# Kernel optimization log

Measured on AMD Instinct MI355X. Metric: run time of the kernel, lower is better.

## Reference

```python
import jax, jax.numpy as jnp
import numpy as np
from jax import lax

B, C, D, H, W = 4, 384, 16, 16, 16
DSTATE, DCONV, EXPAND = 16, 4, 2
DIN = C * EXPAND            # 768
DTRANK = (C + 15) // 16     # 24
EPS = 1e-5


def setup_inputs() -> dict:
    ks = jax.random.split(jax.random.key(0), 12)
    g = lambda k, shape, s=0.02: jax.random.normal(k, shape, jnp.float32) * s
    return {
        "x": jax.random.normal(ks[0], (B, C, D, H, W), jnp.float32),
        "gsc_w1": g(ks[1], (C, C, 3, 3, 3)), "gsc_b1": jnp.zeros((C,), jnp.float32),
        "gsc_w2": g(ks[2], (C, C, 3, 3, 3)), "gsc_b2": jnp.zeros((C,), jnp.float32),
        "gsc_w3": g(ks[3], (C, C, 1, 1, 1)), "gsc_b3": jnp.zeros((C,), jnp.float32),
        "gsc_w4": g(ks[4], (C, C, 1, 1, 1)), "gsc_b4": jnp.zeros((C,), jnp.float32),
        "ln_g": jnp.ones((C,), jnp.float32), "ln_b": jnp.zeros((C,), jnp.float32),
        "in_proj_w": g(ks[5], (2 * DIN, C)),
        "conv1d_w": g(ks[6], (DIN, 1, DCONV), 0.1), "conv1d_b": jnp.zeros((DIN,), jnp.float32),
        "x_proj_w": g(ks[7], (DTRANK + 2 * DSTATE, DIN)),
        "dt_proj_w": g(ks[8], (DIN, DTRANK), 0.1), "dt_proj_b": jnp.full((DIN,), -4.0, jnp.float32),
        "A_log": jnp.log(jnp.tile(jnp.arange(1, DSTATE + 1, dtype=jnp.float32), (DIN, 1))),
        "D_skip": jnp.ones((DIN,), jnp.float32),
        "out_proj_w": g(ks[9], (C, DIN)),
    }


def _conv3d(x, w, b, pad):
    y = lax.conv_general_dilated(x, w, (1, 1, 1), [(pad, pad)] * 3,
                                 dimension_numbers=("NCDHW", "OIDHW", "NCDHW"))
    return y + b[None, :, None, None, None]


def _inorm(x):  # InstanceNorm3d, affine=False, biased variance
    m = x.mean((2, 3, 4), keepdims=True)
    v = x.var((2, 3, 4), keepdims=True)
    return (x - m) * lax.rsqrt(v + EPS)


def _forward(x, gsc_w1, gsc_b1, gsc_w2, gsc_b2, gsc_w3, gsc_b3, gsc_w4, gsc_b4,
             ln_g, ln_b, in_proj_w, conv1d_w, conv1d_b, x_proj_w,
             dt_proj_w, dt_proj_b, A_log, D_skip, out_proj_w):
    relu = jax.nn.relu
    # ---- GSC block (residual gated spatial conv) ----
    x1 = relu(_inorm(_conv3d(x, gsc_w1, gsc_b1, 1)))
    x1 = relu(_inorm(_conv3d(x1, gsc_w2, gsc_b2, 1)))
    x2 = relu(_inorm(_conv3d(x, gsc_w3, gsc_b3, 0)))
    xg = relu(_inorm(_conv3d(x1 + x2, gsc_w4, gsc_b4, 0))) + x
    # ---- MambaLayer: flatten voxels to tokens ----
    Bn = xg.shape[0]
    L = D * H * W
    t = xg.reshape(Bn, C, L).swapaxes(1, 2)                     # [B, L, C]
    mu = t.mean(-1, keepdims=True)
    var = t.var(-1, keepdims=True)
    tn = (t - mu) * lax.rsqrt(var + EPS) * ln_g + ln_b          # LayerNorm
    # ---- Mamba block ----
    xz = tn @ in_proj_w.T                                       # [B, L, 2*DIN]
    xin, z = jnp.split(xz, 2, axis=-1)
    xc = xin.swapaxes(1, 2)                                     # [B, DIN, L]
    xc = lax.conv_general_dilated(xc, conv1d_w, (1,), [(DCONV - 1, 0)],
                                  dimension_numbers=("NCH", "OIH", "NCH"),
                                  feature_group_count=DIN)      # causal depthwise conv
    u = jax.nn.silu(xc + conv1d_b[None, :, None]).swapaxes(1, 2)  # [B, L, DIN]
    dbl = u @ x_proj_w.T                                        # [B, L, DTRANK+2N]
    dt, Bm, Cm = jnp.split(dbl, [DTRANK, DTRANK + DSTATE], axis=-1)
    dt = jax.nn.softplus(dt @ dt_proj_w.T + dt_proj_b)          # [B, L, DIN]
    A = -jnp.exp(A_log)                                         # [DIN, N]

    def step(h, inp):  # h: [B, DIN, N]
        dt_t, B_t, C_t, u_t = inp
        dA = jnp.exp(dt_t[:, :, None] * A)
        h = dA * h + (dt_t * u_t)[:, :, None] * B_t[:, None, :]
        return h, jnp.einsum("bdn,bn->bd", h, C_t)

    h0 = jnp.zeros((Bn, DIN, DSTATE), x.dtype)
    _, ys = lax.scan(step, h0, (dt.swapaxes(0, 1), Bm.swapaxes(0, 1),
                                Cm.swapaxes(0, 1), u.swapaxes(0, 1)))
    y = ys.swapaxes(0, 1) + u * D_skip                          # [B, L, DIN]
    y = y * jax.nn.silu(z)
    out = y @ out_proj_w.T                                      # [B, L, C]
    return out.swapaxes(1, 2).reshape(Bn, C, D, H, W)


def reference(x, gsc_w1, gsc_b1, gsc_w2, gsc_b2, gsc_w3, gsc_b3, gsc_w4, gsc_b4,
              ln_g, ln_b, in_proj_w, conv1d_w, conv1d_b, x_proj_w,
              dt_proj_w, dt_proj_b, A_log, D_skip, out_proj_w):
    return _forward(x, gsc_w1, gsc_b1, gsc_w2, gsc_b2, gsc_w3, gsc_b3, gsc_w4, gsc_b4,
                    ln_g, ln_b, in_proj_w, conv1d_w, conv1d_b, x_proj_w,
                    dt_proj_w, dt_proj_b, A_log, D_skip, out_proj_w)
```

## Files before the change

### kernel.cpp

```cpp
#include <hip/hip_runtime.h>
#include <math.h>

#define CDIM 384
#define SDIM 4096
#define BDIM 4
#define DINC 768
#define NST  16
#define NCHUNK 64
#define LCHUNK 64
#define PSTRIDE 6291456

typedef unsigned short ushort_t;
typedef unsigned int uint_t;
typedef __attribute__((ext_vector_type(4))) float f32x4;
typedef __attribute__((ext_vector_type(8))) short bf16x8;

__device__ __forceinline__ ushort_t f2bf(float f) {
    union { float f; uint_t u; } v; v.f = f;
    uint_t r = v.u + 0x7FFFu + ((v.u >> 16) & 1u);
    return (ushort_t)(r >> 16);
}
__device__ __forceinline__ float bf2f(ushort_t u) {
    union { uint_t i; float f; } v; v.i = ((uint_t)u) << 16; return v.f;
}
__device__ __forceinline__ uint_t pk2(float a, float b) {
    return (uint_t)f2bf(a) | ((uint_t)f2bf(b) << 16);
}

__device__ __forceinline__ void wconv_body(const float* __restrict__ W,
                                           ushort_t* __restrict__ Wb, int idx) {
    const float* wp = W + (size_t)idx * 27;
#pragma unroll
    for (int tap = 0; tap < 27; ++tap)
        Wb[(size_t)tap * (CDIM * CDIM) + idx] = f2bf(wp[tap]);
}
__device__ __forceinline__ void cvt_body(const float* __restrict__ src,
                                         ushort_t* __restrict__ dst, int i) {
    float4 v = ((const float4*)src)[i];
    uint2 o; o.x = pk2(v.x, v.y); o.y = pk2(v.z, v.w);
    ((uint2*)dst)[i] = o;
}
__global__ __launch_bounds__(256)
void prep_weights_kernel(const float* w1, const float* w2, const float* w3,
                         const float* w4, const float* ipw, const float* opw,
                         const float* xpw,
                         ushort_t* Wb1, ushort_t* Wb2, ushort_t* w3b, ushort_t* w4b,
                         ushort_t* ipwb, ushort_t* opwb, ushort_t* xpwb) {
    const int bid = blockIdx.x, t = threadIdx.x;
    if      (bid < 576)  wconv_body(w1, Wb1, bid * 256 + t);
    else if (bid < 1152) wconv_body(w2, Wb2, (bid - 576) * 256 + t);
    else if (bid < 1296) cvt_body(w3, w3b, (bid - 1152) * 256 + t);
    else if (bid < 1440) cvt_body(w4, w4b, (bid - 1296) * 256 + t);
    else if (bid < 2016) cvt_body(ipw, ipwb, (bid - 1440) * 256 + t);
    else if (bid < 2304) cvt_body(opw, opwb, (bid - 2016) * 256 + t);
    else                 cvt_body(xpw, xpwb, (bid - 2304) * 256 + t);
}

__global__ __launch_bounds__(384)
void pad_kernel(const float* __restrict__ src, ushort_t* __restrict__ Xp) {
    const int blk = blockIdx.x;
    const int b = blk >> 8, d = (blk >> 4) & 15, h = blk & 15;
    const int ci = threadIdx.x;
    const float* sp = src + (size_t)(b * CDIM + ci) * SDIM + d * 256 + h * 16;
    ushort_t* dp = Xp + ((((size_t)(b * 18 + d + 1) * 18) + (h + 1)) * 18 + 1) * CDIM + ci;
#pragma unroll
    for (int w = 0; w < 16; ++w)
        dp[(size_t)w * CDIM] = f2bf(sp[w]);
}

__global__ __launch_bounds__(384)
void pad_fuse2_kernel(const float* __restrict__ P0, const float* __restrict__ P1,
                      const float* __restrict__ stats, ushort_t* __restrict__ Xp) {
    const int blk = blockIdx.x;
    const int b = blk >> 8, d = (blk >> 4) & 15, h = blk & 15;
    const int ci = threadIdx.x;
    const size_t o = (size_t)(b * CDIM + ci) * SDIM + d * 256 + h * 16;
    const float m = stats[(b * CDIM + ci) * 2], r = stats[(b * CDIM + ci) * 2 + 1];
    ushort_t* dp = Xp + ((((size_t)(b * 18 + d + 1) * 18) + (h + 1)) * 18 + 1) * CDIM + ci;
#pragma unroll
    for (int w = 0; w < 16; ++w) {
        const float v = P0[o + w] + P1[o + w];
        dp[(size_t)w * CDIM] = f2bf(fmaxf((v - m) * r, 0.f));
    }
}

__global__ __launch_bounds__(384)
void pad_fuse3_kernel(const float* __restrict__ P0, const float* __restrict__ P1,
                      const float* __restrict__ st2, const float* __restrict__ C3,
                      const float* __restrict__ st3, ushort_t* __restrict__ Xp) {
    const int blk = blockIdx.x;
    const int b = blk >> 8, d = (blk >> 4) & 15, h = blk & 15;
    const int ci = threadIdx.x;
    const size_t o = (size_t)(b * CDIM + ci) * SDIM + d * 256 + h * 16;
    const float m2 = st2[(b * CDIM + ci) * 2], r2 = st2[(b * CDIM + ci) * 2 + 1];
    const float m3 = st3[(b * CDIM + ci) * 2], r3 = st3[(b * CDIM + ci) * 2 + 1];
    ushort_t* dp = Xp + ((((size_t)(b * 18 + d + 1) * 18) + (h + 1)) * 18 + 1) * CDIM + ci;
#pragma unroll
    for (int w = 0; w < 16; ++w) {
        const float x1 = fmaxf((P0[o + w] + P1[o + w] - m2) * r2, 0.f);
        const float x2 = fmaxf((C3[o + w] - m3) * r3, 0.f);
        dp[(size_t)w * CDIM] = f2bf(x1 + x2);
    }
}

template<int MODE>
__global__ __launch_bounds__(256)
void conv_kernel(const ushort_t* __restrict__ Xp, const ushort_t* __restrict__ Wb,
                 const ushort_t* __restrict__ W3, float* __restrict__ Y01,
                 float* __restrict__ Y2) {
    constexpr int NZ = (MODE == 0) ? 2 : (MODE == 1 ? 3 : 1);
    const int cpx = gridDim.x >> 3;
    const int lin = blockIdx.x;
    const int wid = (lin & 7) * cpx + (lin >> 3);
    const int co0 = (wid % 3) * 128;
    const int zz  = (wid / 3) % NZ;
    const int ntid = wid / (3 * NZ);
    const int b  = ntid >> 5;
    const int d  = (ntid >> 1) & 15;
    const int h0 = (ntid & 1) * 8;
    const int t = threadIdx.x;
    const int lane = t & 63;
    const int wy = (t >> 6) >> 1, wx = (t >> 6) & 1;

    const bool is1x1 = (MODE == 2) || (MODE == 1 && zz == 2);
    const ushort_t* Wsrc; int tap0, iters, kd0, kh0, kw0; float* Y;
    if (is1x1) {
        Wsrc = W3; tap0 = 0; iters = 12; kd0 = 1; kh0 = 1; kw0 = 1; Y = Y2;
    } else {
        Wsrc = Wb; tap0 = zz ? 14 : 0; iters = (zz ? 13 : 14) * 12;
        kd0 = zz ? 1 : 0; kh0 = zz ? 1 : 0; kw0 = zz ? 2 : 0;
        Y = Y01 + (size_t)zz * PSTRIDE;
    }

    __shared__ ushort_t As[2][128 * 40];
    __shared__ ushort_t Bs[2][128 * 40];

    f32x4 acc[4][4];
#pragma unroll
    for (int i = 0; i < 4; ++i)
#pragma unroll
        for (int j = 0; j < 4; ++j) acc[i][j] = (f32x4){0.f, 0.f, 0.f, 0.f};

    const int arow = t >> 1, half = t & 1;
    const int hl = arow >> 4, w = arow & 15;
    const int wA = arow * 40 + half * 16;

    const int lm = lane & 15, lk = (lane >> 4) * 8;
    const int rA0 = (wy * 64 + lm) * 40 + lk;
    const int rB0 = (wx * 64 + lm) * 40 + lk;

    const ushort_t* ap = Wsrc + (size_t)tap0 * (CDIM * CDIM)
                       + (size_t)(co0 + arow) * CDIM + half * 16;
    const ushort_t* bp = Xp + ((((size_t)(b * 18 + d + kd0) * 18) + (h0 + hl + kh0)) * 18
                               + (w + kw0)) * CDIM + half * 16;
    int c12 = 0, ckw = kw0, ckh = kh0;

    uint4 ra0, ra1, rb0, rb1;

    auto loadg = [&]() {
        const uint4* pa = reinterpret_cast<const uint4*>(ap);
        ra0 = pa[0]; ra1 = pa[1];
        const uint4* pb = reinterpret_cast<const uint4*>(bp);
        rb0 = pb[0]; rb1 = pb[1];
        ap += 32; bp += 32;
        if (++c12 == 12) {
            c12 = 0;
            ap += CDIM * CDIM - 384;
            if (++ckw == 3) {
                ckw = 0;
                if (++ckh == 3) { ckh = 0; bp += 109440; }
                else bp += 5760;
            }
        }
    };
    auto lwrite = [&](int buf) {
        *reinterpret_cast<uint4*>(&As[buf][wA])     = ra0;
        *reinterpret_cast<uint4*>(&As[buf][wA + 8]) = ra1;
        *reinterpret_cast<uint4*>(&Bs[buf][wA])     = rb0;
        *reinterpret_cast<uint4*>(&Bs[buf][wA + 8]) = rb1;
    };

    loadg();
    lwrite(0);
    __syncthreads();

    int buf = 0;
    for (int idx = 0; idx < iters; ++idx) {
        const bool more = (idx + 1) < iters;
        if (more) loadg();
        bf16x8 af[4], bfr[4];
#pragma unroll
        for (int mi = 0; mi < 4; ++mi)
            af[mi] = *reinterpret_cast<const bf16x8*>(&As[buf][rA0 + mi * 640]);
#pragma unroll
        for (int ni = 0; ni < 4; ++ni)
            bfr[ni] = *reinterpret_cast<const bf16x8*>(&Bs[buf][rB0 + ni * 640]);
#pragma unroll
        for (int mi = 0; mi < 4; ++mi)
#pragma unroll
            for (int ni = 0; ni < 4; ++ni)
                acc[mi][ni] = __builtin_amdgcn_mfma_f32_16x16x32_bf16(
                    af[mi], bfr[ni], acc[mi][ni], 0, 0, 0);
        if (more) lwrite(buf ^ 1);
        __syncthreads();
        buf ^= 1;
    }

    const int coB = co0 + wy * 64 + (lane >> 4) * 4;
    const int nB  = wx * 64 + lm;
#pragma unroll
    for (int mi = 0; mi < 4; ++mi) {
#pragma unroll
        for (int ni = 0; ni < 4; ++ni) {
            const int nl = nB + ni * 16;
            const int s = d * 256 + (h0 + (nl >> 4)) * 16 + (nl & 15);
            float* yp = Y + ((size_t)b * CDIM + (coB + mi * 16)) * SDIM + s;
#pragma unroll
            for (int j = 0; j < 4; ++j)
                yp[(size_t)j * SDIM] = acc[mi][ni][j];
        }
    }
}

template<int EPI>
__global__ __launch_bounds__(256)
void gemm_mfma_kernel(const ushort_t* __restrict__ A, const ushort_t* __restrict__ Bw,
                      void* __restrict__ Cv, void* __restrict__ C2v,
                      int M, int N, int K, int ldc, int nx) {
    const int cpx = gridDim.x >> 3;
    const int lin = blockIdx.x;
    const int wid = (lin & 7) * cpx + (lin >> 3);
    const int n0 = (wid % nx) * 128;
    const int m0 = (wid / nx) * 128;
    const int t = threadIdx.x;
    const int lane = t & 63;
    const int wy = (t >> 6) >> 1, wx = (t >> 6) & 1;

    __shared__ ushort_t As[2][128 * 40];
    __shared__ ushort_t Bs[2][128 * 40];

    f32x4 acc[4][4];
#pragma unroll
    for (int i = 0; i < 4; ++i)
#pragma unroll
        for (int j = 0; j < 4; ++j) acc[i][j] = (f32x4){0.f, 0.f, 0.f, 0.f};

    const int arow = t >> 1, half = t & 1;
    const int wA = arow * 40 + half * 16;
    const int lm = lane & 15, lk = (lane >> 4) * 8;
    const int rA0 = (wy * 64 + lm) * 40 + lk;
    const int rB0 = (wx * 64 + lm) * 40 + lk;

    uint4 ra0, ra1, rb0, rb1;

    auto loadg = [&](int kk) {
        const int kb = kk * 32 + half * 16;
        const uint4* pa = reinterpret_cast<const uint4*>(
            A + (size_t)(m0 + arow) * K + kb);
        ra0 = pa[0]; ra1 = pa[1];
        if (n0 + arow < N) {
            const uint4* pb = reinterpret_cast<const uint4*>(
                Bw + (size_t)(n0 + arow) * K + kb);
            rb0 = pb[0]; rb1 = pb[1];
        } else {
            rb0 = make_uint4(0, 0, 0, 0); rb1 = rb0;
        }
    };
    auto lwrite = [&](int buf) {
        *reinterpret_cast<uint4*>(&As[buf][wA])     = ra0;
        *reinterpret_cast<uint4*>(&As[buf][wA + 8]) = ra1;
        *reinterpret_cast<uint4*>(&Bs[buf][wA])     = rb0;
        *reinterpret_cast<uint4*>(&Bs[buf][wA + 8]) = rb1;
    };

    const int KI = K >> 5;
    loadg(0);
    lwrite(0);
    __syncthreads();

    int buf = 0;
    for (int kk = 0; kk < KI; ++kk) {
        const bool more = (kk + 1) < KI;
        if (more) loadg(kk + 1);
        bf16x8 af[4], bfr[4];
#pragma unroll
        for (int mi = 0; mi < 4; ++mi)
            af[mi] = *reinterpret_cast<const bf16x8*>(&As[buf][rA0 + mi * 640]);
#pragma unroll
        for (int ni = 0; ni < 4; ++ni)
            bfr[ni] = *reinterpret_cast<const bf16x8*>(&Bs[buf][rB0 + ni * 640]);
#pragma unroll
        for (int mi = 0; mi < 4; ++mi)
#pragma unroll
            for (int ni = 0; ni < 4; ++ni)
                acc[mi][ni] = __builtin_amdgcn_mfma_f32_16x16x32_bf16(
                    af[mi], bfr[ni], acc[mi][ni], 0, 0, 0);
        if (more) lwrite(buf ^ 1);
        __syncthreads();
        buf ^= 1;
    }

    const int mB = m0 + wy * 64 + (lane >> 4) * 4;
    const int nB = n0 + wx * 64 + lm;
#pragma unroll
    for (int mi = 0; mi < 4; ++mi) {
#pragma unroll
        for (int ni = 0; ni < 4; ++ni) {
            const int n = nB + ni * 16;
            if (EPI == 2) {
                const int mrow = mB + mi * 16;
                const int bb = mrow >> 12, l = mrow & 4095;
                float4 st = {acc[mi][ni][0], acc[mi][ni][1],
                             acc[mi][ni][2], acc[mi][ni][3]};
                *reinterpret_cast<float4*>(
                    (float*)Cv + ((size_t)(bb * CDIM + n)) * SDIM + l) = st;
            } else {
#pragma unroll
                for (int j = 0; j < 4; ++j) {
                    const int m = mB + mi * 16 + j;
                    const float v = acc[mi][ni][j];
                    if (EPI == 0) {
                        if (n < N) ((float*)Cv)[(size_t)m * ldc + n] = v;
                    } else {
                        if (n < DINC) ((ushort_t*)Cv)[(size_t)m * DINC + n] = f2bf(v);
                        else ((ushort_t*)C2v)[(size_t)m * DINC + (n - DINC)] = f2bf(v);
                    }
                }
            }
        }
    }
}

__device__ __forceinline__ void stats_reduce(float s, float ss, float* out) {
#pragma unroll
    for (int off = 32; off > 0; off >>= 1) {
        s += __shfl_down(s, off);
        ss += __shfl_down(ss, off);
    }
    __shared__ float rs[4], rss[4];
    const int wid = threadIdx.x >> 6;
    if ((threadIdx.x & 63) == 0) { rs[wid] = s; rss[wid] = ss; }
    __syncthreads();
    if (threadIdx.x == 0) {
        float S = rs[0] + rs[1] + rs[2] + rs[3];
        float SS = rss[0] + rss[1] + rss[2] + rss[3];
        float m = S * (1.f / SDIM);
        float var = SS * (1.f / SDIM) - m * m;
        out[0] = m;
        out[1] = rsqrtf(var + 1e-5f);
    }
}

__global__ __launch_bounds__(256)
void inorm_stats_combo_kernel(const float* __restrict__ P0, const float* __restrict__ P1,
                              float* __restrict__ SA, const float* __restrict__ X3,
                              float* __restrict__ SB) {
    const int bid = blockIdx.x;
    float s = 0.f, ss = 0.f;
    if (bid < 1536) {
        const float* p0 = P0 + (size_t)bid * SDIM;
        const float* p1 = P1 + (size_t)bid * SDIM;
        for (int i = threadIdx.x * 4; i < SDIM; i += 1024) {
            float4 a = *(const float4*)(p0 + i);
            float4 c = *(const float4*)(p1 + i);
            const float vx = a.x + c.x, vy = a.y + c.y, vz = a.z + c.z, vw = a.w + c.w;
            s += vx + vy + vz + vw;
            ss += vx * vx + vy * vy + vz * vz + vw * vw;
        }
        stats_reduce(s, ss, SA + bid * 2);
    } else {
        const int bc = bid - 1536;
        const float* xp = X3 + (size_t)bc * SDIM;
        for (int i = threadIdx.x * 4; i < SDIM; i += 1024) {
            float4 v = *(const float4*)(xp + i);
            s += v.x + v.y + v.z + v.w;
            ss += v.x * v.x + v.y * v.y + v.z * v.z + v.w * v.w;
        }
        stats_reduce(s, ss, SB + bc * 2);
    }
}

__global__ __launch_bounds__(256)
void inorm_stats_kernel(const float* __restrict__ X, float* __restrict__ stats) {
    const int bc = blockIdx.x;
    const float* xp = X + (size_t)bc * SDIM;
    float s = 0.f, ss = 0.f;
    for (int i = threadIdx.x * 4; i < SDIM; i += 1024) {
        float4 v = *(const float4*)(xp + i);
        s += v.x + v.y + v.z + v.w;
        ss += v.x * v.x + v.y * v.y + v.z * v.z + v.w * v.w;
    }
    stats_reduce(s, ss, stats + bc * 2);
}

__global__ __launch_bounds__(256)
void layernorm_kernel(const float* __restrict__ C4, const float* __restrict__ stats,
                      const float* __restrict__ X, const float* __restrict__ gam,
                      const float* __restrict__ bet, ushort_t* __restrict__ Tn) {
    const int token = blockIdx.x * 4 + (threadIdx.x >> 6);
    const int lane = threadIdx.x & 63;
    const int b = token >> 12, l = token & 4095;
    const size_t base = (size_t)b * CDIM * SDIM + l;
    float v[6];
    float s = 0.f, ss = 0.f;
#pragma unroll
    for (int i = 0; i < 6; ++i) {
        const int c = lane + i * 64;
        const size_t o = base + (size_t)c * SDIM;
        const float m = stats[(b * CDIM + c) * 2], r = stats[(b * CDIM + c) * 2 + 1];
        v[i] = fmaxf((C4[o] - m) * r, 0.f) + X[o];
        s += v[i]; ss += v[i] * v[i];
    }
#pragma unroll
    for (int off = 32; off > 0; off >>= 1) {
        s += __shfl_down(s, off);
        ss += __shfl_down(ss, off);
    }
    s = __shfl(s, 0); ss = __shfl(ss, 0);
    const float m = s * (1.f / CDIM);
    const float r = rsqrtf(ss * (1.f / CDIM) - m * m + 1e-5f);
    ushort_t* tp = Tn + (size_t)token * CDIM;
#pragma unroll
    for (int i = 0; i < 6; ++i) {
        const int c = lane + i * 64;
        tp[c] = f2bf((v[i] - m) * r * gam[c] + bet[c]);
    }
}

__global__ __launch_bounds__(256)
void gemm_dtproj_kernel(const float* __restrict__ A, const float* __restrict__ B,
                        ushort_t* __restrict__ C, const float* __restrict__ bias,
                        int M, int N, int K, int lda, int ldb, int ldc) {
    __shared__ __align__(16) float As[16][132];
    __shared__ __align__(16) float Bs[16][68];
    const int t = threadIdx.x;
    const int m0 = blockIdx.y * 128;
    const int n0 = blockIdx.x * 64;

    float acc[8][4];
#pragma unroll
    for (int i = 0; i < 8; ++i)
#pragma unroll
        for (int j = 0; j < 4; ++j) acc[i][j] = 0.f;

    const int mr = (t & 15) * 8;
    const int nr = (t >> 4) * 4;

    for (int k0 = 0; k0 < K; k0 += 16) {
#pragma unroll
        for (int idx = 0; idx < 8; ++idx) {
            const int e = idx * 256 + t;
            const int k = e & 15, m = e >> 4;
            float v = 0.f;
            if (k0 + k < K) v = A[(size_t)(m0 + m) * lda + (k0 + k)];
            As[k][m] = v;
        }
#pragma unroll
        for (int idx = 0; idx < 4; ++idx) {
            const int e = idx * 256 + t;
            const int k = e & 15, n = e >> 4;
            float v = 0.f;
            if ((n0 + n) < N && (k0 + k) < K) v = B[(size_t)(n0 + n) * ldb + (k0 + k)];
            Bs[k][n] = v;
        }
        __syncthreads();
#pragma unroll
        for (int k = 0; k < 16; ++k) {
            float4 a0 = *(const float4*)&As[k][mr];
            float4 a1 = *(const float4*)&As[k][mr + 4];
            float4 b0 = *(const float4*)&Bs[k][nr];
            const float av[8] = {a0.x, a0.y, a0.z, a0.w, a1.x, a1.y, a1.z, a1.w};
            const float bv[4] = {b0.x, b0.y, b0.z, b0.w};
#pragma unroll
            for (int i = 0; i < 8; ++i)
#pragma unroll
                for (int j = 0; j < 4; ++j)
                    acc[i][j] = fmaf(av[i], bv[j], acc[i][j]);
        }
        __syncthreads();
    }

#pragma unroll
    for (int i = 0; i < 8; ++i) {
        const int m = m0 + mr + i;
#pragma unroll
        for (int j = 0; j < 4; ++j) {
            const int n = n0 + nr + j;
            if (n >= N) continue;
            float v = acc[i][j] + bias[n];
            v = (v > 20.f) ? v : log1pf(__expf(v));
            C[(size_t)m * ldc + n] = f2bf(v);
        }
    }
}

__global__ __launch_bounds__(256)
void dwconv_silu_kernel(const ushort_t* __restrict__ Xin, const float* __restrict__ W,
                        const float* __restrict__ bias, ushort_t* __restrict__ U) {
    const int dch = blockIdx.x * 256 + threadIdx.x;
    const int l0 = blockIdx.y * 4, b = blockIdx.z;
    const float4 w4 = ((const float4*)W)[dch];
    const float wk[4] = {w4.x, w4.y, w4.z, w4.w};
    const float bs = bias[dch];
    const size_t base = ((size_t)b * 4096 + l0) * DINC + dch;
    float r[7];
#pragma unroll
    for (int k = 0; k < 7; ++k) {
        const int ll = l0 - 3 + k;
        r[k] = (ll >= 0) ? bf2f(Xin[base + (size_t)(k - 3) * DINC]) : 0.f;
    }
#pragma unroll
    for (int j = 0; j < 4; ++j) {
        float acc = bs;
#pragma unroll
        for (int k = 0; k < 4; ++k) acc = fmaf(r[j + k], wk[k], acc);
        U[base + (size_t)j * DINC] = f2bf(acc / (1.f + __expf(-acc)));
    }
}

__global__ __launch_bounds__(256)
void scan_phase1_kernel(const ushort_t* __restrict__ DT, const ushort_t* __restrict__ U,
                        const float* __restrict__ DBL, const float* __restrict__ A_log,
                        float* __restrict__ HOUT, float* __restrict__ SDT) {
    const int b = blockIdx.z, chunk = blockIdx.y;
    const int dch = blockIdx.x * 256 + threadIdx.x;
    float Arow[16];
#pragma unroll
    for (int n = 0; n < NST; ++n) Arow[n] = -__expf(A_log[dch * NST + n]);

    __shared__ float bcs[LCHUNK][16];
    const size_t tokbase = (size_t)b * 4096 + chunk * LCHUNK;
#pragma unroll
    for (int idx = 0; idx < 4; ++idx) {
        const int e = idx * 256 + threadIdx.x;
        bcs[e >> 4][e & 15] = DBL[(tokbase + (e >> 4)) * 56 + 24 + (e & 15)];
    }
    __syncthreads();

    size_t off = tokbase * DINC + dch;
    float h[16];
#pragma unroll
    for (int n = 0; n < NST; ++n) h[n] = 0.f;
    float sdt = 0.f;
    float cdt = bf2f(DT[off]), cu = bf2f(U[off]);
    for (int t = 0; t < LCHUNK; ++t) {
        float ndt = 0.f, nu = 0.f;
        if (t < LCHUNK - 1) { ndt = bf2f(DT[off + DINC]); nu = bf2f(U[off + DINC]); }
        sdt += cdt;
        const float du = cdt * cu;
#pragma unroll
        for (int n = 0; n < NST; ++n)
            h[n] = __expf(cdt * Arow[n]) * h[n] + du * bcs[t][n];
        off += DINC;
        cdt = ndt; cu = nu;
    }
    float* hp = HOUT + (((size_t)(b * DINC + dch) * NCHUNK + chunk) << 4);
#pragma unroll
    for (int n = 0; n < NST; ++n) hp[n] = h[n];
    SDT[(size_t)(b * DINC + dch) * NCHUNK + chunk] = sdt;
}

__global__ __launch_bounds__(256)
void scan_phase2_kernel(float* __restrict__ HOUT, const float* __restrict__ SDT,
                        const float* __restrict__ A_log) {
    const int t = blockIdx.x * 256 + threadIdx.x;
    const int b = t / (DINC * NST);
    const int rem = t - b * (DINC * NST);
    const int d = rem >> 4, n = rem & 15;
    const float An = -__expf(A_log[d * NST + n]);
    float* hp = HOUT + (((size_t)(b * DINC + d) * NCHUNK) << 4) + n;
    const float* sp = SDT + (size_t)(b * DINC + d) * NCHUNK;
    float H = 0.f;
    for (int c = 0; c < NCHUNK; ++c) {
        const float tmp = hp[c * 16];
        const float dA = __expf(An * sp[c]);
        hp[c * 16] = H;
        H = dA * H + tmp;
    }
}

__global__ __launch_bounds__(256)
void scan_phase3_kernel(ushort_t* __restrict__ DT, const ushort_t* __restrict__ U,
                        const float* __restrict__ DBL, const ushort_t* __restrict__ Z,
                        const float* __restrict__ A_log, const float* __restrict__ D_skip,
                        const float* __restrict__ HOUT) {
    const int b = blockIdx.z, chunk = blockIdx.y;
    const int dch = blockIdx.x * 256 + threadIdx.x;
    float Arow[16];
#pragma unroll
    for (int n = 0; n < NST; ++n) Arow[n] = -__expf(A_log[dch * NST + n]);
    const float Dsk = D_skip[dch];

    __shared__ float bcs[LCHUNK][32];
    const size_t tokbase = (size_t)b * 4096 + chunk * LCHUNK;
#pragma unroll
    for (int idx = 0; idx < 8; ++idx) {
        const int e = idx * 256 + threadIdx.x;
        bcs[e >> 5][e & 31] = DBL[(tokbase + (e >> 5)) * 56 + 24 + (e & 31)];
    }
    __syncthreads();

    float h[16];
    const float* hp = HOUT + (((size_t)(b * DINC + dch) * NCHUNK + chunk) << 4);
#pragma unroll
    for (int n = 0; n < NST; ++n) h[n] = hp[n];

    size_t off = tokbase * DINC + dch;
    float cdt = bf2f(DT[off]), cu = bf2f(U[off]), cz = bf2f(Z[off]);
    for (int t = 0; t < LCHUNK; ++t) {
        float ndt = 0.f, nu = 0.f, nz = 0.f;
        if (t < LCHUNK - 1) {
            ndt = bf2f(DT[off + DINC]); nu = bf2f(U[off + DINC]); nz = bf2f(Z[off + DINC]);
        }
        const float du = cdt * cu;
        float y = 0.f;
#pragma unroll
        for (int n = 0; n < NST; ++n) {
            h[n] = __expf(cdt * Arow[n]) * h[n] + du * bcs[t][n];
            y = fmaf(h[n], bcs[t][16 + n], y);
        }
        y += cu * Dsk;
        const float sz = cz / (1.f + __expf(-cz));
        DT[off] = f2bf(y * sz);
        off += DINC;
        cdt = ndt; cu = nu; cz = nz;
    }
}

extern "C" void kernel_launch(void* const* d_in, const int* in_sizes, int n_in,
                              void* d_out, int out_size, void* d_ws, size_t ws_size,
                              hipStream_t stream) {
    (void)in_sizes; (void)n_in; (void)out_size; (void)ws_size;
    const float* x         = (const float*)d_in[0];
    const float* w1        = (const float*)d_in[1];
    const float* w2        = (const float*)d_in[3];
    const float* w3        = (const float*)d_in[5];
    const float* w4        = (const float*)d_in[7];
    const float* ln_g      = (const float*)d_in[9];
    const float* ln_b      = (const float*)d_in[10];
    const float* in_proj_w = (const float*)d_in[11];
    const float* conv1d_w  = (const float*)d_in[12];
    const float* conv1d_b  = (const float*)d_in[13];
    const float* x_proj_w  = (const float*)d_in[14];
    const float* dt_proj_w = (const float*)d_in[15];
    const float* dt_proj_b = (const float*)d_in[16];
    const float* A_log     = (const float*)d_in[17];
    const float* D_skip    = (const float*)d_in[18];
    const float* out_proj_w= (const float*)d_in[19];
    float* out = (float*)d_out;

    float* ws = (float*)d_ws;
    float* R0 = ws;
    float* R1 = ws + 6291456;
    float* R2 = ws + 12582912;
    float* R3 = ws + 25165824;
    float* R4 = ws + 37748736;

    float*    P0    = R0;
    float*    P1    = R1;
    ushort_t* Wb1   = (ushort_t*)R2;
    ushort_t* Xp    = (ushort_t*)(R2 + 2097152);
    ushort_t* w3b   = (ushort_t*)(R2 + 6576128);
    ushort_t* w4b   = (ushort_t*)(R2 + 6649856);
    ushort_t* Wb2   = (ushort_t*)(R2 + 6723584);
    float*    SA    = R4;
    float*    SB    = R4 + 4096;
    ushort_t* ipwb  = (ushort_t*)(R4 + 6291456);
    ushort_t* opwb  = (ushort_t*)(R4 + 6586368);
    ushort_t* xpwb  = (ushort_t*)(R4 + 6733824);
    ushort_t* tnb   = (ushort_t*)R0;
    float*    DBL   = R0 + 3145728;
    float*    HOUT  = R1;
    float*    SDT   = R1 + 3145728;
    ushort_t* XIN   = (ushort_t*)R2;
    ushort_t* Zb    = (ushort_t*)R3;
    ushort_t* Ub    = (ushort_t*)R4;
    ushort_t* DTb   = (ushort_t*)R2;

    const size_t XP_BYTES = (size_t)4 * 18 * 18 * 18 * CDIM * 2;

    hipMemsetAsync(Xp, 0, XP_BYTES, stream);
    prep_weights_kernel<<<2346, 256, 0, stream>>>(
        w1, w2, w3, w4, in_proj_w, out_proj_w, x_proj_w,
        Wb1, Wb2, w3b, w4b, ipwb, opwb, xpwb);
    pad_kernel<<<1024, 384, 0, stream>>>(x, Xp);
    conv_kernel<1><<<1152, 256, 0, stream>>>(Xp, Wb1, w3b, P0, R3);
    inorm_stats_combo_kernel<<<3072, 256, 0, stream>>>(P0, P1, SA, R3, SB);
    pad_fuse2_kernel<<<1024, 384, 0, stream>>>(P0, P1, SA, Xp);
    conv_kernel<0><<<768, 256, 0, stream>>>(Xp, Wb2, nullptr, P0, nullptr);
    inorm_stats_combo_kernel<<<1536, 256, 0, stream>>>(P0, P1, SA, nullptr, nullptr);
    pad_fuse3_kernel<<<1024, 384, 0, stream>>>(P0, P1, SA, R3, SB, Xp);
    conv_kernel<2><<<384, 256, 0, stream>>>(Xp, nullptr, w4b, nullptr, R3);
    inorm_stats_kernel<<<1536, 256, 0, stream>>>(R3, SA);
    layernorm_kernel<<<4096, 256, 0, stream>>>(R3, SA, x, ln_g, ln_b, tnb);
    gemm_mfma_kernel<1><<<1536, 256, 0, stream>>>(
        tnb, ipwb, XIN, Zb, 16384, 1536, CDIM, 0, 12);
    dwconv_silu_kernel<<<dim3(3, 1024, 4), 256, 0, stream>>>(XIN, conv1d_w, conv1d_b, Ub);
    gemm_mfma_kernel<0><<<128, 256, 0, stream>>>(
        Ub, xpwb, DBL, nullptr, 16384, 56, DINC, 56, 1);
    gemm_dtproj_kernel<<<dim3(12, 128), 256, 0, stream>>>(
        DBL, dt_proj_w, DTb, dt_proj_b, 16384, DINC, 24, 56, 24, DINC);
    scan_phase1_kernel<<<dim3(3, NCHUNK, 4), 256, 0, stream>>>(
        DTb, Ub, DBL, A_log, HOUT, SDT);
    scan_phase2_kernel<<<192, 256, 0, stream>>>(HOUT, SDT, A_log);
    scan_phase3_kernel<<<dim3(3, NCHUNK, 4), 256, 0, stream>>>(
        DTb, Ub, DBL, Zb, A_log, D_skip, HOUT);
    gemm_mfma_kernel<2><<<384, 256, 0, stream>>>(
        DTb, opwb, out, nullptr, 16384, CDIM, DINC, 0, 3);
}
```

Baseline: 892.1 us.

## Load conv tiles directly into LDS with swizzle, drop XCD block remap

The implicit-GEMM conv kernel now uses global_load_lds to copy A and B tiles straight into a single-buffered, XOR-swizzled LDS tile with no padding, replacing register-staged double buffering. Blocks are reordered so spatial tiles vary fastest, and the XCD-aware block remapping is removed from both the conv and GEMM kernels. This cuts VGPR pressure and LDS footprint, which may raise occupancy. It also gives up the overlap of global loads with MFMA work inside a block and adds a second barrier per iteration.

Result: faster. 810.2 us (-9.2%).

```diff
diff --git a/kernel.cpp b/kernel.cpp
--- a/kernel.cpp
+++ b/kernel.cpp
@@ -25,6 +25,11 @@
 }
 __device__ __forceinline__ uint_t pk2(float a, float b) {
     return (uint_t)f2bf(a) | ((uint_t)f2bf(b) << 16);
+}
+__device__ __forceinline__ void gl16(const ushort_t* g, ushort_t* l) {
+    __builtin_amdgcn_global_load_lds(
+        (const __attribute__((address_space(1))) void*)(g),
+        (__attribute__((address_space(3))) void*)(l), 16, 0, 0);
 }
 
 __device__ __forceinline__ void wconv_body(const float* __restrict__ W,
@@ -108,19 +113,18 @@
 void conv_kernel(const ushort_t* __restrict__ Xp, const ushort_t* __restrict__ Wb,
                  const ushort_t* __restrict__ W3, float* __restrict__ Y01,
                  float* __restrict__ Y2) {
-    constexpr int NZ = (MODE == 0) ? 2 : (MODE == 1 ? 3 : 1);
-    const int cpx = gridDim.x >> 3;
-    const int lin = blockIdx.x;
-    const int wid = (lin & 7) * cpx + (lin >> 3);
-    const int co0 = (wid % 3) * 128;
-    const int zz  = (wid / 3) % NZ;
-    const int ntid = wid / (3 * NZ);
+    const int wid = blockIdx.x;
+    const int ntid = wid & 127;
+    const int rest = wid >> 7;
+    const int co0 = (rest % 3) * 128;
+    const int zz  = rest / 3;
     const int b  = ntid >> 5;
     const int d  = (ntid >> 1) & 15;
     const int h0 = (ntid & 1) * 8;
     const int t = threadIdx.x;
     const int lane = t & 63;
-    const int wy = (t >> 6) >> 1, wx = (t >> 6) & 1;
+    const int wv = t >> 6;
+    const int wy = wv >> 1, wx = wv & 1;
 
     const bool is1x1 = (MODE == 2) || (MODE == 1 && zz == 2);
     const ushort_t* Wsrc; int tap0, iters, kd0, kh0, kw0; float* Y;
@@ -132,8 +136,8 @@
         Y = Y01 + (size_t)zz * PSTRIDE;
     }
 
-    __shared__ ushort_t As[2][128 * 40];
-    __shared__ ushort_t Bs[2][128 * 40];
+    __shared__ __align__(16) ushort_t As[4096];
+    __shared__ __align__(16) ushort_t Bs[4096];
 
     f32x4 acc[4][4];
 #pragma unroll
@@ -141,69 +145,58 @@
 #pragma unroll
         for (int j = 0; j < 4; ++j) acc[i][j] = (f32x4){0.f, 0.f, 0.f, 0.f};
 
-    const int arow = t >> 1, half = t & 1;
-    const int hl = arow >> 4, w = arow & 15;
-    const int wA = arow * 40 + half * 16;
-
-    const int lm = lane & 15, lk = (lane >> 4) * 8;
-    const int rA0 = (wy * 64 + lm) * 40 + lk;
-    const int rB0 = (wx * 64 + lm) * 40 + lk;
-
-    const ushort_t* ap = Wsrc + (size_t)tap0 * (CDIM * CDIM)
-                       + (size_t)(co0 + arow) * CDIM + half * 16;
-    const ushort_t* bp = Xp + ((((size_t)(b * 18 + d + kd0) * 18) + (h0 + hl + kh0)) * 18
-                               + (w + kw0)) * CDIM + half * 16;
+    const int l4 = lane >> 2;
+    const int cg = (((lane & 3) ^ ((lane >> 3) & 3)) << 3);
+    int aTC[2], bTC[2];
+#pragma unroll
+    for (int i = 0; i < 2; ++i) {
+        const int r = wv * 32 + i * 16 + l4;
+        aTC[i] = (co0 + r) * CDIM + cg;
+        bTC[i] = ((r >> 4) * 18 + (r & 15)) * CDIM + cg;
+    }
+    ushort_t* lA[2] = { &As[wv * 1024], &As[wv * 1024 + 512] };
+    ushort_t* lB[2] = { &Bs[wv * 1024], &Bs[wv * 1024 + 512] };
+
+    int aoff = tap0 * (CDIM * CDIM);
+    int goff = (((b * 18 + d + kd0) * 18 + (h0 + kh0)) * 18 + kw0) * CDIM;
     int c12 = 0, ckw = kw0, ckh = kh0;
 
-    uint4 ra0, ra1, rb0, rb1;
-
-    auto loadg = [&]() {
-        const uint4* pa = reinterpret_cast<const uint4*>(ap);
-        ra0 = pa[0]; ra1 = pa[1];
-        const uint4* pb = reinterpret_cast<const uint4*>(bp);
-        rb0 = pb[0]; rb1 = pb[1];
-        ap += 32; bp += 32;
+    const int lm = lane & 15;
+    const int sw8 = (((lane >> 4) ^ ((lm >> 1) & 3)) << 3);
+    const int rA0 = (wy * 64 + lm) * 32 + sw8;
+    const int rB0 = (wx * 64 + lm) * 32 + sw8;
+
+    for (int idx = 0; idx < iters; ++idx) {
+#pragma unroll
+        for (int i = 0; i < 2; ++i) {
+            gl16(Wsrc + aoff + aTC[i], lA[i]);
+            gl16(Xp + goff + bTC[i], lB[i]);
+        }
+        aoff += 32; goff += 32;
         if (++c12 == 12) {
             c12 = 0;
-            ap += CDIM * CDIM - 384;
+            aoff += CDIM * CDIM - CDIM;
             if (++ckw == 3) {
                 ckw = 0;
-                if (++ckh == 3) { ckh = 0; bp += 109440; }
-                else bp += 5760;
+                if (++ckh == 3) { ckh = 0; goff += 109440; }
+                else goff += 5760;
             }
         }
-    };
-    auto lwrite = [&](int buf) {
-        *reinterpret_cast<uint4*>(&As[buf][wA])     = ra0;
-        *reinterpret_cast<uint4*>(&As[buf][wA + 8]) = ra1;
-        *reinterpret_cast<uint4*>(&Bs[buf][wA])     = rb0;
-        *reinterpret_cast<uint4*>(&Bs[buf][wA + 8]) = rb1;
-    };
-
-    loadg();
-    lwrite(0);
-    __syncthreads();
-
-    int buf = 0;
-    for (int idx = 0; idx < iters; ++idx) {
-        const bool more = (idx + 1) < iters;
-        if (more) loadg();
+        __syncthreads();
         bf16x8 af[4], bfr[4];
 #pragma unroll
         for (int mi = 0; mi < 4; ++mi)
-            af[mi] = *reinterpret_cast<const bf16x8*>(&As[buf][rA0 + mi * 640]);
+            af[mi] = *reinterpret_cast<const bf16x8*>(&As[rA0 + mi * 512]);
 #pragma unroll
         for (int ni = 0; ni < 4; ++ni)
-            bfr[ni] = *reinterpret_cast<const bf16x8*>(&Bs[buf][rB0 + ni * 640]);
+            bfr[ni] = *reinterpret_cast<const bf16x8*>(&Bs[rB0 + ni * 512]);
 #pragma unroll
         for (int mi = 0; mi < 4; ++mi)
 #pragma unroll
             for (int ni = 0; ni < 4; ++ni)
                 acc[mi][ni] = __builtin_amdgcn_mfma_f32_16x16x32_bf16(
                     af[mi], bfr[ni], acc[mi][ni], 0, 0, 0);
-        if (more) lwrite(buf ^ 1);
         __syncthreads();
-        buf ^= 1;
     }
 
     const int coB = co0 + wy * 64 + (lane >> 4) * 4;
@@ -227,9 +220,7 @@
 void gemm_mfma_kernel(const ushort_t* __restrict__ A, const ushort_t* __restrict__ Bw,
                       void* __restrict__ Cv, void* __restrict__ C2v,
                       int M, int N, int K, int ldc, int nx) {
-    const int cpx = gridDim.x >> 3;
-    const int lin = blockIdx.x;
-    const int wid = (lin & 7) * cpx + (lin >> 3);
+    const int wid = blockIdx.x;
     const int n0 = (wid % nx) * 128;
     const int m0 = (wid / nx) * 128;
     const int t = threadIdx.x;
```
